# Kernel tuning notes

Hardware: AMD Instinct MI355X
Metric: run time of the kernel (lower is better)

## Reference

```python
import jax, jax.numpy as jnp
import numpy as np

N = 8192
HID = 256
LAMBDA = 1.0
MU = 1.0
DIM = 2
GC = 0.0027
L = 0.02
Y0, Y1 = 0.0, 1.0
STRESS_PRE_SCALE = 1.0
PF_PRE_SCALE = 1.0


def loading(t):
    # linear displacement loading
    return t[0]


def mlp(Ws, bs, inp):
    h = inp
    for W, b in zip(Ws[:-1], bs[:-1]):
        h = jnp.tanh(h @ W + b)
    return h @ Ws[-1] + bs[-1]


def net_u(Ws, bs, x, t):
    sol = mlp(Ws, bs, jnp.concatenate([x, t]))  # (3,)
    phi = jax.nn.sigmoid(sol[:1])               # (1,)
    ld = loading(t)
    ux = (x[1] - Y0) * (x[1] - Y1) * sol[1:2] * ld / 3.0
    uy = (x[1] - Y0) * (x[1] - Y1) * sol[2:3] * ld + (x[1] - Y0) / (Y1 - Y0) * ld
    return phi, jnp.concatenate([ux, uy])       # (1,), (2,)


def epsilon_fn(Ws, bs, x, t):
    J = jax.jacrev(lambda xx: net_u(Ws, bs, xx, t)[1])(x)  # (2,2)
    return (J + J.T) / 2.0


def psi_pos(eps):
    tr = jnp.trace(eps)
    k = LAMBDA + MU * 2.0 / DIM
    dev = eps - tr * jnp.eye(DIM, dtype=eps.dtype) / DIM
    return k * jax.nn.relu(tr) ** 2 / 2 + MU * jnp.trace(dev @ dev)


def psi_neg(eps):
    k = LAMBDA + MU * 2.0 / DIM
    return k * jax.nn.relu(-jnp.trace(eps)) ** 2 / 2


def sigma_fn(Ws, bs, x, t):
    phi, _ = net_u(Ws, bs, x, t)
    g_phi = (1 - phi[0]) ** 2 + 1e-6
    eps = epsilon_fn(Ws, bs, x, t)
    return g_phi * jax.grad(psi_pos)(eps) + jax.grad(psi_neg)(eps)


def net_stress(Ws, bs, x, t):
    def damaged(xx):
        phi, _ = net_u(Ws, bs, xx, t)
        return (1 - phi) ** 2 * sigma_fn(Ws, bs, xx, t)  # (2,2)
    D = jax.jacrev(damaged)(x)          # (2,2,2)
    return jnp.einsum('ijj->i', D) / STRESS_PRE_SCALE


def net_pf_raw(Ws, bs, x, t):
    phi, _ = net_u(Ws, bs, x, t)
    phi0 = phi[0]
    eps = epsilon_fn(Ws, bs, x, t)
    H = jax.hessian(lambda xx: net_u(Ws, bs, xx, t)[0])(x)[0]  # (2,2)
    lap_phi = jnp.trace(H)
    pf = GC * (phi0 / L - L * lap_phi) - 2 * (1 - phi0) * psi_pos(eps)
    return pf / PF_PRE_SCALE


def net_speed(Ws, bs, x, t):
    return jax.jacrev(lambda tt: net_u(Ws, bs, x, tt)[0])(t)[0, 0]


def net_pf(Ws, bs, x, t):
    pf = net_pf_raw(Ws, bs, x, t)
    dphi_dt = net_speed(Ws, bs, x, t)
    phi0 = net_u(Ws, bs, x, t)[0][0]
    mask_pos = (jnp.abs(dphi_dt) <= 1e-3) & (jnp.abs(phi0 - 1) > 1e-3)
    mask_neg = jnp.abs(phi0 - 1) <= 1e-3
    return jnp.where(mask_pos, jax.nn.relu(-pf), jnp.where(mask_neg, jax.nn.relu(pf), pf))


def net_energy(Ws, bs, x, t):
    phi0 = net_u(Ws, bs, x, t)[0][0]
    eps = epsilon_fn(Ws, bs, x, t)
    nphi = jax.jacrev(lambda xx: net_u(Ws, bs, xx, t)[0])(x)[0]  # (2,)
    return ((1 - phi0) * 2 * psi_pos(eps) + psi_neg(eps)
            + GC * (phi0 ** 2 / (2 * L) + L / 2 * jnp.sum(nphi ** 2)))


def _forward(W0, W1, W2, W3, W4, b0, b1, b2, b3, b4, x, t):
    Ws = [W0, W1, W2, W3, W4]
    bs = [b0, b1, b2, b3, b4]
    res_s = jax.vmap(net_stress, in_axes=(None, None, 0, 0))(Ws, bs, x, t)   # (N,2)
    res_pf = jax.vmap(net_pf, in_axes=(None, None, 0, 0))(Ws, bs, x, t)     # (N,)
    res_e = jax.vmap(net_energy, in_axes=(None, None, 0, 0))(Ws, bs, x, t)  # (N,)
    dphi = jax.vmap(net_speed, in_axes=(None, None, 0, 0))(Ws, bs, x, t)    # (N,)
    # component re-weighting for the vector stress residual (as in loss_pde)
    mse_res = jnp.mean(res_s ** 2, axis=0)  # (2,)
    w = jax.lax.stop_gradient(jnp.mean(mse_res) / (mse_res + 1e-6))
    r = jnp.sqrt(jnp.sum(res_s ** 2 * w[None, :], axis=-1))
    loss_stress = jnp.mean(r ** 2)
    loss_pf = jnp.mean(res_pf ** 2)
    loss_energy = jnp.log(jnp.sum(res_e))
    loss_irr = jnp.mean(jax.nn.relu(-dphi))
    return jnp.stack([loss_stress, loss_pf, loss_energy, loss_irr])


def setup_inputs() -> dict:
    key = jax.random.key(0)
    dims = [3, HID, HID, HID, HID, 3]
    ks = jax.random.split(key, 12)
    inp = {}
    for i in range(5):
        fan_in, fan_out = dims[i], dims[i + 1]
        inp[f'W{i}'] = (jax.random.normal(ks[i], (fan_in, fan_out), jnp.float32)
                        * np.sqrt(2.0 / (fan_in + fan_out)).astype(np.float32))
        inp[f'b{i}'] = jnp.zeros((fan_out,), jnp.float32)
    inp['x'] = jax.random.uniform(ks[10], (N, 2), jnp.float32, 0.0, 1.0)
    inp['t'] = jax.random.uniform(ks[11], (N, 1), jnp.float32, 0.05, 1.0)
    return inp


def reference(W0, W1, W2, W3, W4, b0, b1, b2, b3, b4, x, t):
    return _forward(W0, W1, W2, W3, W4, b0, b1, b2, b3, b4, x, t)
```

## Files before the change

kernel.cpp:

```cpp
#include <hip/hip_runtime.h>
#include <math.h>

#define N_PTS 8192
#define HIDDEN 256
#define PPB 8
#define THREADS 256
#define NBLK (N_PTS / PPB)
#define NBINS 64
#define MROWS 56
#define LDA 264
#define LDZ 260
#define BP_OFF 4096

typedef float f32x4 __attribute__((ext_vector_type(4)));
typedef short s8v  __attribute__((ext_vector_type(8)));
typedef short s4v  __attribute__((ext_vector_type(4)));

__device__ __forceinline__ unsigned short bf16_rne(float x) {
    unsigned int u = __float_as_uint(x);
    return (unsigned short)((u + 0x7FFFu + ((u >> 16) & 1u)) >> 16);
}
__device__ __forceinline__ float bf16f(unsigned short h) {
    return __uint_as_float(((unsigned int)h) << 16);
}

__global__ void pinn_pack(const float* __restrict__ W1, const float* __restrict__ W2,
                          const float* __restrict__ W3, unsigned short* __restrict__ Bp,
                          float* __restrict__ bins)
{
    if (blockIdx.x == 0) {
        bins[threadIdx.x] = 0.f;
        bins[threadIdx.x + 256] = 0.f;
    }
    const int id = blockIdx.x * 256 + threadIdx.x;
    const int lane = id & 63;
    const int nt   = (id >> 6) & 15;
    const int kc   = (id >> 10) & 7;
    const int l    = id >> 13;
    const float* W = (l == 0) ? W1 : ((l == 1) ? W2 : W3);
    const int n  = nt * 16 + (lane & 15);
    const int k0 = kc * 32 + (lane >> 4) * 8;
    unsigned short hi[8], lo[8];
    #pragma unroll
    for (int i = 0; i < 8; ++i) {
        const float x = W[(size_t)(k0 + i) * HIDDEN + n];
        const unsigned short h = bf16_rne(x);
        hi[i] = h;
        lo[i] = bf16_rne(x - bf16f(h));
    }
    const size_t bh = ((((size_t)(l * 2 + 0) * 8 + kc) * 16 + nt) * 64 + lane) * 8;
    const size_t bl = ((((size_t)(l * 2 + 1) * 8 + kc) * 16 + nt) * 64 + lane) * 8;
    *(s8v*)&Bp[bh] = *(const s8v*)hi;
    *(s8v*)&Bp[bl] = *(const s8v*)lo;
}

__global__ __launch_bounds__(THREADS, 2)
void pinn_main(const float* __restrict__ W0, const float* __restrict__ b0,
               const float* __restrict__ b1, const float* __restrict__ b2,
               const float* __restrict__ b3,
               const float* __restrict__ W4, const float* __restrict__ b4,
               const float* __restrict__ xin, const float* __restrict__ tin,
               const unsigned short* __restrict__ Bp,
               float* __restrict__ bins)
{
    __shared__ __align__(16) unsigned char LB[MROWS * LDA * 4];
    short* __restrict__ AhS = (short*)LB;
    short* __restrict__ AlS = (short*)(LB + MROWS * LDA * 2);
    float* __restrict__ Zf  = (float*)LB;

    const int tid  = threadIdx.x;
    const int lane = tid & 63;
    const int w    = tid >> 6;
    const int c    = lane & 15;
    const int g    = lane >> 4;
    const int q    = tid & 63;
    const int pp   = tid >> 6;
    const int pt0  = blockIdx.x * PPB;

    {
        const f32x4 w0 = *(const f32x4*)(W0 + q * 4);
        const f32x4 w1 = *(const f32x4*)(W0 + HIDDEN + q * 4);
        const f32x4 w2 = *(const f32x4*)(W0 + 2 * HIDDEN + q * 4);
        const f32x4 bb = *(const f32x4*)(b0 + q * 4);
        #pragma unroll
        for (int p2 = 0; p2 < 2; ++p2) {
            const int p = pp + 4 * p2;
            const float x0 = xin[(pt0 + p) * 2 + 0];
            const float x1 = xin[(pt0 + p) * 2 + 1];
            const float tt = tin[pt0 + p];
            s4v hi[7], lo[7];
            #pragma unroll
            for (int jj = 0; jj < 4; ++jj) {
                const float z  = fmaf(x0, w0[jj], fmaf(x1, w1[jj], fmaf(tt, w2[jj], bb[jj])));
                const float a  = tanhf(z);
                const float st = 1.f - a * a;
                const float m2 = -2.f * a * st;
                float v[7];
                v[0] = a;
                v[1] = st * w0[jj]; v[2] = st * w1[jj]; v[3] = st * w2[jj];
                v[4] = m2 * w0[jj] * w0[jj];
                v[5] = m2 * w0[jj] * w1[jj];
                v[6] = m2 * w1[jj] * w1[jj];
                #pragma unroll
                for (int s = 0; s < 7; ++s) {
                    const unsigned short h = bf16_rne(v[s]);
                    hi[s][jj] = (short)h;
                    lo[s][jj] = (short)bf16_rne(v[s] - bf16f(h));
                }
            }
            #pragma unroll
            for (int s = 0; s < 7; ++s) {
                const int r = 8 * s + p;
                *(s4v*)&AhS[r * LDA + q * 4] = hi[s];
                *(s4v*)&AlS[r * LDA + q * 4] = lo[s];
            }
        }
    }
    __syncthreads();

    int aoff[4];
    #pragma unroll
    for (int mt = 0; mt < 4; ++mt) {
        int arow = mt * 16 + c;
        if (arow > MROWS - 1) arow = MROWS - 1;
        aoff[mt] = arow * LDA + g * 8;
    }

    for (int l = 0; l < 3; ++l) {
        f32x4 acc[4][4];
        #pragma unroll
        for (int mt = 0; mt < 4; ++mt)
            #pragma unroll
            for (int nn = 0; nn < 4; ++nn) acc[mt][nn] = (f32x4)0.f;

        const size_t lbase = (size_t)l * 2 * 8 * 16 * 64 * 8;
        #pragma unroll
        for (int kc = 0; kc < 8; ++kc) {
            s8v ah[4], al[4];
            #pragma unroll
            for (int mt = 0; mt < 4; ++mt) {
                ah[mt] = *(const s8v*)&AhS[aoff[mt] + kc * 32];
                al[mt] = *(const s8v*)&AlS[aoff[mt] + kc * 32];
            }
            s8v bh[4], bl[4];
            #pragma unroll
            for (int nn = 0; nn < 4; ++nn) {
                const int nt = w * 4 + nn;
                const size_t oh = lbase + (((size_t)kc * 16 + nt) * 64 + lane) * 8;
                const size_t ol = oh + (size_t)8 * 16 * 64 * 8;
                bh[nn] = *(const s8v*)&Bp[oh];
                bl[nn] = *(const s8v*)&Bp[ol];
            }
            #pragma unroll
            for (int mt = 0; mt < 4; ++mt)
                #pragma unroll
                for (int nn = 0; nn < 4; ++nn) {
                    acc[mt][nn] = __builtin_amdgcn_mfma_f32_16x16x32_bf16(ah[mt], bh[nn], acc[mt][nn], 0, 0, 0);
                    acc[mt][nn] = __builtin_amdgcn_mfma_f32_16x16x32_bf16(ah[mt], bl[nn], acc[mt][nn], 0, 0, 0);
                    acc[mt][nn] = __builtin_amdgcn_mfma_f32_16x16x32_bf16(al[mt], bh[nn], acc[mt][nn], 0, 0, 0);
                }
        }
        __syncthreads();

        #pragma unroll
        for (int mt = 0; mt < 4; ++mt)
            #pragma unroll
            for (int nn = 0; nn < 4; ++nn)
                #pragma unroll
                for (int r = 0; r < 4; ++r) {
                    const int row = mt * 16 + g * 4 + r;
                    if (row < MROWS)
                        Zf[row * LDZ + w * 64 + nn * 16 + c] = acc[mt][nn][r];
                }
        __syncthreads();

        f32x4 z[2][7];
        #pragma unroll
        for (int p2 = 0; p2 < 2; ++p2) {
            const int p = pp + 4 * p2;
            #pragma unroll
            for (int s = 0; s < 7; ++s)
                z[p2][s] = *(const f32x4*)&Zf[(8 * s + p) * LDZ + q * 4];
        }
        __syncthreads();

        const float* bias = (l == 0) ? b1 : (l == 1) ? b2 : b3;
        const f32x4 bb = *(const f32x4*)(bias + q * 4);
        #pragma unroll
        for (int p2 = 0; p2 < 2; ++p2) {
            const int p = pp + 4 * p2;
            s4v hi[7], lo[7];
            f32x4 vf[7];
            #pragma unroll
            for (int jj = 0; jj < 4; ++jj) {
                const float zv = z[p2][0][jj] + bb[jj];
                const float a  = tanhf(zv);
                const float st = 1.f - a * a;
                const float m2 = -2.f * a * st;
                const float z1 = z[p2][1][jj], z2 = z[p2][2][jj], z3 = z[p2][3][jj];
                float v[7];
                v[0] = a;
                v[1] = st * z1; v[2] = st * z2; v[3] = st * z3;
                v[4] = fmaf(m2 * z1, z1, st * z[p2][4][jj]);
                v[5] = fmaf(m2 * z1, z2, st * z[p2][5][jj]);
                v[6] = fmaf(m2 * z2, z2, st * z[p2][6][jj]);
                if (l < 2) {
                    #pragma unroll
                    for (int s = 0; s < 7; ++s) {
                        const unsigned short h = bf16_rne(v[s]);
                        hi[s][jj] = (short)h;
                        lo[s][jj] = (short)bf16_rne(v[s] - bf16f(h));
                    }
                } else {
                    #pragma unroll
                    for (int s = 0; s < 7; ++s) vf[s][jj] = v[s];
                }
            }
            if (l < 2) {
                #pragma unroll
                for (int s = 0; s < 7; ++s) {
                    const int r = 8 * s + p;
                    *(s4v*)&AhS[r * LDA + q * 4] = hi[s];
                    *(s4v*)&AlS[r * LDA + q * 4] = lo[s];
                }
            } else {
                #pragma unroll
                for (int s = 0; s < 7; ++s)
                    *(f32x4*)&Zf[(8 * s + p) * LDZ + q * 4] = vf[s];
            }
        }
        __syncthreads();
    }

    const int h  = (lane >> 5);
    const int la = lane & 31;
    const int p  = w * 2 + h;

    float part[7][3];
    #pragma unroll
    for (int s = 0; s < 7; ++s)
        #pragma unroll
        for (int m = 0; m < 3; ++m) part[s][m] = 0.f;

    #pragma unroll
    for (int i = 0; i < 8; ++i) {
        const int k = la + 32 * i;
        const float w40 = W4[k * 3 + 0], w41 = W4[k * 3 + 1], w42 = W4[k * 3 + 2];
        #pragma unroll
        for (int s = 0; s < 7; ++s) {
            const float hk = Zf[(8 * s + p) * LDZ + k];
            part[s][0] = fmaf(hk, w40, part[s][0]);
            part[s][1] = fmaf(hk, w41, part[s][1]);
            part[s][2] = fmaf(hk, w42, part[s][2]);
        }
    }
    #pragma unroll
    for (int s = 0; s < 7; ++s)
        #pragma unroll
        for (int m = 0; m < 3; ++m) {
            float v = part[s][m];
            #pragma unroll
            for (int off = 16; off > 0; off >>= 1) v += __shfl_xor(v, off);
            part[s][m] = v;
        }

    const float x0 = xin[(pt0 + p) * 2 + 0];
    const float x1 = xin[(pt0 + p) * 2 + 1];
    const float tt = tin[pt0 + p];

    const float V0 = part[0][0] + b4[0];
    const float V1 = part[0][1] + b4[1];
    const float V2 = part[0][2] + b4[2];
    const float J00 = part[1][0], J01 = part[2][0], J0t = part[3][0];
    const float J10 = part[1][1], J11 = part[2][1];
    const float J20 = part[1][2], J21 = part[2][2];
    const float H000 = part[4][0], H011 = part[6][0];
    const float H100 = part[4][1], H101 = part[5][1], H111 = part[6][1];
    const float H200 = part[4][2], H201 = part[5][2], H211 = part[6][2];

    const float phi = 1.f / (1.f + expf(-V0));
    const float om  = 1.f - phi;
    const float sp  = phi * om;
    const float spp = sp * (1.f - 2.f * phi);
    const float phx0 = sp * J00, phx1 = sp * J01, dphidt = sp * J0t;
    const float lap = spp * (J00 * J00 + J01 * J01) + sp * (H000 + H011);

    const float ld = tt;
    const float qq = x1 * (x1 - 1.f), qp = 2.f * x1 - 1.f;

    const float ux0 = qq * J10 * ld * (1.f / 3.f);
    const float ux1 = (qp * V1 + qq * J11) * ld * (1.f / 3.f);
    const float uy0 = qq * J20 * ld;
    const float uy1 = (qp * V2 + qq * J21) * ld + ld;

    const float e00 = ux0, e11 = uy1, e01 = 0.5f * (ux1 + uy0);
    const float tr = e00 + e11;

    const float ux_00 = qq * H100 * ld * (1.f / 3.f);
    const float ux_01 = (qp * J10 + qq * H101) * ld * (1.f / 3.f);
    const float ux_11 = (2.f * V1 + 2.f * qp * J11 + qq * H111) * ld * (1.f / 3.f);
    const float uy_00 = qq * H200 * ld;
    const float uy_01 = (qp * J20 + qq * H201) * ld;
    const float uy_11 = (2.f * V2 + 2.f * qp * J21 + qq * H211) * ld;

    const float de00_0 = ux_00, de00_1 = ux_01;
    const float de11_0 = uy_01, de11_1 = uy_11;
    const float de01_0 = 0.5f * (ux_01 + uy_00), de01_1 = 0.5f * (ux_11 + uy_01);
    const float dtr_0 = de00_0 + de11_0, dtr_1 = de00_1 + de11_1;

    const float kk = 2.f;
    const float rtr = fmaxf(tr, 0.f), rntr = fmaxf(-tr, 0.f);
    const float Hp = (tr > 0.f) ? 1.f : 0.f, Hn = (tr < 0.f) ? 1.f : 0.f;

    const float dv = 0.5f * (e00 - e11);
    const float sp00 = kk * rtr + 2.f * dv;
    const float sp11 = kk * rtr - 2.f * dv;
    const float sp01 = 2.f * e01;
    const float snd  = -kk * rntr;

    const float dsp00_0 = kk * Hp * dtr_0 + 2.f * (de00_0 - 0.5f * dtr_0);
    const float dsp01_0 = 2.f * de01_0;
    const float dsp01_1 = 2.f * de01_1;
    const float dsp11_1 = kk * Hp * dtr_1 + 2.f * (de11_1 - 0.5f * dtr_1);
    const float dsn_0 = kk * Hn * dtr_0, dsn_1 = kk * Hn * dtr_1;

    const float cc  = om * om, gg = cc + 1e-6f;
    const float dc0 = -2.f * om * phx0, dc1 = -2.f * om * phx1;
    const float gpc = gg + cc, cg = cc * gg;

    const float res0 = dc0 * gpc * sp00 + cg * dsp00_0 + dc0 * snd + cc * dsn_0
                     + dc1 * gpc * sp01 + cg * dsp01_1;
    const float res1 = dc0 * gpc * sp01 + cg * dsp01_0
                     + dc1 * gpc * sp11 + cg * dsp11_1 + dc1 * snd + cc * dsn_1;

    const float psip = rtr * rtr + 0.5f * (e00 - e11) * (e00 - e11) + 2.f * e01 * e01;
    const float psin = rntr * rntr;

    const float GCc = 0.0027f, LL = 0.02f;
    const float pf = GCc * (phi / LL - LL * lap) - 2.f * om * psip;
    const bool maskp = (fabsf(dphidt) <= 1e-3f) && (fabsf(phi - 1.f) > 1e-3f);
    const bool maskn = fabsf(phi - 1.f) <= 1e-3f;
    const float respf = maskp ? fmaxf(-pf, 0.f) : (maskn ? fmaxf(pf, 0.f) : pf);

    const float rese = om * 2.f * psip + psin
                     + GCc * (phi * phi / (2.f * LL)
                              + 0.5f * LL * (phx0 * phx0 + phx1 * phx1));
    const float irr = fmaxf(-dphidt, 0.f);

    if (la == 0) {
        float* bin = bins + (blockIdx.x & (NBINS - 1)) * 8;
        atomicAdd(bin + 0, res0 * res0);
        atomicAdd(bin + 1, res1 * res1);
        atomicAdd(bin + 2, respf * respf);
        atomicAdd(bin + 3, rese);
        atomicAdd(bin + 4, irr);
    }
}

__global__ void pinn_finalize(const float* __restrict__ bins, float* __restrict__ out)
{
    const int lane = threadIdx.x;
    float s0 = bins[lane * 8 + 0];
    float s1 = bins[lane * 8 + 1];
    float s2 = bins[lane * 8 + 2];
    float s3 = bins[lane * 8 + 3];
    float s4 = bins[lane * 8 + 4];
    #pragma unroll
    for (int off = 32; off > 0; off >>= 1) {
        s0 += __shfl_xor(s0, off);
        s1 += __shfl_xor(s1, off);
        s2 += __shfl_xor(s2, off);
        s3 += __shfl_xor(s3, off);
        s4 += __shfl_xor(s4, off);
    }
    if (lane == 0) {
        const float inv_n = 1.f / (float)N_PTS;
        const float mse0 = s0 * inv_n, mse1 = s1 * inv_n;
        const float wm = 0.5f * (mse0 + mse1);
        out[0] = wm * mse0 / (mse0 + 1e-6f) + wm * mse1 / (mse1 + 1e-6f);
        out[1] = s2 * inv_n;
        out[2] = logf(s3);
        out[3] = s4 * inv_n;
    }
}

extern "C" void kernel_launch(void* const* d_in, const int* in_sizes, int n_in,
                              void* d_out, int out_size, void* d_ws, size_t ws_size,
                              hipStream_t stream)
{
    const float *W[5], *b[5];
    if (in_sizes[1] == HIDDEN) {
        for (int i = 0; i < 5; ++i) {
            W[i] = (const float*)d_in[2 * i];
            b[i] = (const float*)d_in[2 * i + 1];
        }
    } else {
        for (int i = 0; i < 5; ++i) {
            W[i] = (const float*)d_in[i];
            b[i] = (const float*)d_in[5 + i];
        }
    }
    const float* x = (const float*)d_in[10];
    const float* t = (const float*)d_in[11];
    float* bins = (float*)d_ws;
    unsigned short* Bp = (unsigned short*)((char*)d_ws + BP_OFF);

    pinn_pack<<<96, 256, 0, stream>>>(W[1], W[2], W[3], Bp, bins);
    pinn_main<<<NBLK, THREADS, 0, stream>>>(W[0], b[0], b[1], b[2], b[3],
                                            W[4], b[4], x, t, Bp, bins);
    pinn_finalize<<<1, 64, 0, stream>>>(bins, (float*)d_out);
}
```

Baseline: 161.6 us.

## Epilogue in MFMA registers via permuted row/K layout; fuse finalize kernel

Rows of the A tile are reordered so each lane's MFMA accumulator holds all seven derivative streams for its own points. The tanh and derivative epilogue therefore runs directly on accumulators, which removes the Zf store/reload round trip and two barriers per layer. The weight K dimension is permuted in the pack kernel and in the W4 readout so the new column order stays consistent. The separate finalize launch is replaced by a last-block-done atomic counter inside the main kernel, which adds extra LDS and a global atomic per block.

```diff
diff --git a/kernel.cpp b/kernel.cpp
--- a/kernel.cpp
+++ b/kernel.cpp
@@ -7,9 +7,9 @@
 #define THREADS 256
 #define NBLK (N_PTS / PPB)
 #define NBINS 64
-#define MROWS 56
 #define LDA 264
-#define LDZ 260
+#define AROWS 62
+#define LDZ 264
 #define BP_OFF 4096
 
 typedef float f32x4 __attribute__((ext_vector_type(4)));
@@ -22,6 +22,10 @@
 }
 __device__ __forceinline__ float bf16f(unsigned short h) {
     return __uint_as_float(((unsigned int)h) << 16);
+}
+__device__ __forceinline__ int rowof(int s, int p) {
+    return (s < 6) ? ((s >> 1) * 16 + (p >> 1) * 4 + (p & 1) * 2 + (s & 1))
+                   : (48 + (p >> 1) * 4 + (p & 1));
 }
 
 __global__ void pinn_pack(const float* __restrict__ W1, const float* __restrict__ W2,
@@ -31,6 +35,7 @@
     if (blockIdx.x == 0) {
         bins[threadIdx.x] = 0.f;
         bins[threadIdx.x + 256] = 0.f;
+        if (threadIdx.x == 0) *(unsigned*)(bins + 512) = 0u;
     }
     const int id = blockIdx.x * 256 + threadIdx.x;
     const int lane = id & 63;
@@ -39,11 +44,12 @@
     const int l    = id >> 13;
     const float* W = (l == 0) ? W1 : ((l == 1) ? W2 : W3);
     const int n  = nt * 16 + (lane & 15);
-    const int k0 = kc * 32 + (lane >> 4) * 8;
     unsigned short hi[8], lo[8];
     #pragma unroll
     for (int i = 0; i < 8; ++i) {
-        const float x = W[(size_t)(k0 + i) * HIDDEN + n];
+        const int kslot = kc * 32 + (lane >> 4) * 8 + i;
+        const int korig = ((kslot >> 6) & 3) * 64 + (kslot & 3) * 16 + ((kslot >> 2) & 15);
+        const float x = W[(size_t)korig * HIDDEN + n];
         const unsigned short h = bf16_rne(x);
         hi[i] = h;
         lo[i] = bf16_rne(x - bf16f(h));
@@ -61,11 +67,11 @@
                const float* __restrict__ W4, const float* __restrict__ b4,
                const float* __restrict__ xin, const float* __restrict__ tin,
                const unsigned short* __restrict__ Bp,
-               float* __restrict__ bins)
+               float* __restrict__ bins, float* __restrict__ out)
 {
-    __shared__ __align__(16) unsigned char LB[MROWS * LDA * 4];
+    __shared__ __align__(16) unsigned char LB[65472];
     short* __restrict__ AhS = (short*)LB;
-    short* __restrict__ AlS = (short*)(LB + MROWS * LDA * 2);
+    short* __restrict__ AlS = (short*)(LB + AROWS * LDA * 2);
     float* __restrict__ Zf  = (float*)LB;
 
     const int tid  = threadIdx.x;
@@ -73,58 +79,70 @@
     const int w    = tid >> 6;
     const int c    = lane & 15;
     const int g    = lane >> 4;
-    const int q    = tid & 63;
-    const int pp   = tid >> 6;
     const int pt0  = blockIdx.x * PPB;
+    unsigned* cnt  = (unsigned*)(bins + 512);
 
     {
-        const f32x4 w0 = *(const f32x4*)(W0 + q * 4);
-        const f32x4 w1 = *(const f32x4*)(W0 + HIDDEN + q * 4);
-        const f32x4 w2 = *(const f32x4*)(W0 + 2 * HIDDEN + q * 4);
-        const f32x4 bb = *(const f32x4*)(b0 + q * 4);
-        #pragma unroll
-        for (int p2 = 0; p2 < 2; ++p2) {
-            const int p = pp + 4 * p2;
+        const int c0i = tid & 15, w0i = (tid >> 4) & 3, pp = tid >> 6;
+        float w0v[4], w1v[4], w2v[4], bbv[4];
+        #pragma unroll
+        for (int nn = 0; nn < 4; ++nn) {
+            const int j = w0i * 64 + 16 * nn + c0i;
+            w0v[nn] = W0[j]; w1v[nn] = W0[HIDDEN + j]; w2v[nn] = W0[2 * HIDDEN + j];
+            bbv[nn] = b0[j];
+        }
+        const int sbase = 4 * (c0i + 16 * w0i);
+        #pragma unroll
+        for (int e = 0; e < 2; ++e) {
+            const int p = pp + 4 * e;
             const float x0 = xin[(pt0 + p) * 2 + 0];
             const float x1 = xin[(pt0 + p) * 2 + 1];
             const float tt = tin[pt0 + p];
             s4v hi[7], lo[7];
             #pragma unroll
-            for (int jj = 0; jj < 4; ++jj) {
-                const float z  = fmaf(x0, w0[jj], fmaf(x1, w1[jj], fmaf(tt, w2[jj], bb[jj])));
+            for (int nn = 0; nn < 4; ++nn) {
+                const float z  = fmaf(x0, w0v[nn], fmaf(x1, w1v[nn], fmaf(tt, w2v[nn], bbv[nn])));
                 const float a  = tanhf(z);
                 const float st = 1.f - a * a;
                 const float m2 = -2.f * a * st;
                 float v[7];
                 v[0] = a;
-                v[1] = st * w0[jj]; v[2] = st * w1[jj]; v[3] = st * w2[jj];
-                v[4] = m2 * w0[jj] * w0[jj];
-                v[5] = m2 * w0[jj] * w1[jj];
-                v[6] = m2 * w1[jj] * w1[jj];
+                v[1] = st * w0v[nn]; v[2] = st * w1v[nn]; v[3] = st * w2v[nn];
+                v[4] = m2 * w0v[nn] * w0v[nn];
+                v[5] = m2 * w0v[nn] * w1v[nn];
+                v[6] = m2 * w1v[nn] * w1v[nn];
                 #pragma unroll
                 for (int s = 0; s < 7; ++s) {
                     const unsigned short h = bf16_rne(v[s]);
-                    hi[s][jj] = (short)h;
-                    lo[s][jj] = (short)bf16_rne(v[s] - bf16f(h));
+                    hi[s][nn] = (short)h;
+                    lo[s][nn] = (short)bf16_rne(v[s] - bf16f(h));
                 }
             }
             #pragma unroll
             for (int s = 0; s < 7; ++s) {
-                const int r = 8 * s + p;
-                *(s4v*)&AhS[r * LDA + q * 4] = hi[s];
-                *(s4v*)&AlS[r * LDA + q * 4] = lo[s];
-            }
+                const int r = rowof(s, p);
+                *(s4v*)&AhS[r * LDA + sbase] = hi[s];
+                *(s4v*)&AlS[r * LDA + sbase] = lo[s];
+            }
+        }
+        if (pp == 0) {
+            const s4v z4 = {0, 0, 0, 0};
+            #pragma unroll
+            for (int b = 0; b < 3; ++b)
+                #pragma unroll
+                for (int d = 2; d < 4; ++d) {
+                    const int r = 48 + 4 * b + d;
+                    *(s4v*)&AhS[r * LDA + sbase] = z4;
+                    *(s4v*)&AlS[r * LDA + sbase] = z4;
+                }
         }
     }
     __syncthreads();
 
     int aoff[4];
     #pragma unroll
-    for (int mt = 0; mt < 4; ++mt) {
-        int arow = mt * 16 + c;
-        if (arow > MROWS - 1) arow = MROWS - 1;
-        aoff[mt] = arow * LDA + g * 8;
-    }
+    for (int mt = 0; mt < 3; ++mt) aoff[mt] = (16 * mt + c) * LDA + g * 8;
+    aoff[3] = (48 + ((c >= 14) ? 0 : c)) * LDA + g * 8;
 
     for (int l = 0; l < 3; ++l) {
         f32x4 acc[4][4];
@@ -162,71 +180,54 @@
         }
         __syncthreads();
 
-        #pragma unroll
-        for (int mt = 0; mt < 4; ++mt)
-            #pragma unroll
-            for (int nn = 0; nn < 4; ++nn)
-                #pragma unroll
-                for (int r = 0; r < 4; ++r) {
-                    const int row = mt * 16 + g * 4 + r;
-                    if (row < MROWS)
-                        Zf[row * LDZ + w * 64 + nn * 16 + c] = acc[mt][nn][r];
-                }
-        __syncthreads();
-
-        f32x4 z[2][7];
-        #pragma unroll
-        for (int p2 = 0; p2 < 2; ++p2) {
-            const int p = pp + 4 * p2;
-            #pragma unroll
-            for (int s = 0; s < 7; ++s)
-                z[p2][s] = *(const f32x4*)&Zf[(8 * s + p) * LDZ + q * 4];
-        }
-        __syncthreads();
-
         const float* bias = (l == 0) ? b1 : (l == 1) ? b2 : b3;
-        const f32x4 bb = *(const f32x4*)(bias + q * 4);
-        #pragma unroll
-        for (int p2 = 0; p2 < 2; ++p2) {
-            const int p = pp + 4 * p2;
-            s4v hi[7], lo[7];
-            f32x4 vf[7];
-            #pragma unroll
-            for (int jj = 0; jj < 4; ++jj) {
-                const float zv = z[p2][0][jj] + bb[jj];
-                const float a  = tanhf(zv);
+        float bbv[4];
+        #pragma unroll
+        for (int nn = 0; nn < 4; ++nn) bbv[nn] = bias[64 * w + 16 * nn + c];
+        const int sbase = 4 * (c + 16 * w);
+
+        #pragma unroll
+        for (int e = 0; e < 2; ++e) {
+            const int p = 2 * g + e;
+            float v[7][4];
+            #pragma unroll
+            for (int nn = 0; nn < 4; ++nn) {
+                const float z0 = acc[0][nn][2 * e + 0] + bbv[nn];
+                const float z1 = acc[0][nn][2 * e + 1];
+                const float z2 = acc[1][nn][2 * e + 0];
+                const float z3 = acc[1][nn][2 * e + 1];
+                const float z4 = acc[2][nn][2 * e + 0];
+                const float z5 = acc[2][nn][2 * e + 1];
+                const float z6 = acc[3][nn][e];
+                const float a  = tanhf(z0);
                 const float st = 1.f - a * a;
                 const float m2 = -2.f * a * st;
-                const float z1 = z[p2][1][jj], z2 = z[p2][2][jj], z3 = z[p2][3][jj];
-                float v[7];
-                v[0] = a;
-                v[1] = st * z1; v[2] = st * z2; v[3] = st * z3;
-                v[4] = fmaf(m2 * z1, z1, st * z[p2][4][jj]);
-                v[5] = fmaf(m2 * z1, z2, st * z[p2][5][jj]);
-                v[6] = fmaf(m2 * z2, z2, st * z[p2][6][jj]);
-                if (l < 2) {
-                    #pragma unroll
-                    for (int s = 0; s < 7; ++s) {
-                        const unsigned short h = bf16_rne(v[s]);
-                        hi[s][jj] = (short)h;
-                        lo[s][jj] = (short)bf16_rne(v[s] - bf16f(h));
-                    }
-                } else {
-                    #pragma unroll
-                    for (int s = 0; s < 7; ++s) vf[s][jj] = v[s];
-                }
+                v[0][nn] = a;
+                v[1][nn] = st * z1; v[2][nn] = st * z2; v[3][nn] = st * z3;
+                v[4][nn] = fmaf(m2 * z1, z1, st * z4);
+                v[5][nn] = fmaf(m2 * z1, z2, st * z5);
+                v[6][nn] = fmaf(m2 * z2, z2, st * z6);
             }
             if (l < 2) {
                 #pragma unroll
                 for (int s = 0; s < 7; ++s) {
-                    const int r = 8 * s + p;
-                    *(s4v*)&AhS[r * LDA + q * 4] = hi[s];
-                    *(s4v*)&AlS[r * LDA + q * 4] = lo[s];
+                    s4v hi, lo;
+                    #pragma unroll
+                    for (int nn = 0; nn < 4; ++nn) {
+                        const unsigned short h = bf16_rne(v[s][nn]);
+                        hi[nn] = (short)h;
+                        lo[nn] = (short)bf16_rne(v[s][nn] - bf16f(h));
+                    }
+                    const int r = rowof(s, p);
+                    *(s4v*)&AhS[r * LDA + sbase] = hi;
+                    *(s4v*)&AlS[r * LDA + sbase] = lo;
                 }
             } else {
                 #pragma unroll
-                for (int s = 0; s < 7; ++s)
-                    *(f32x4*)&Zf[(8 * s + p) * LDZ + q * 4] = vf[s];
+                for (int s = 0; s < 7; ++s) {
+                    f32x4 vv = {v[s][0], v[s][1], v[s][2], v[s][3]};
+                    *(f32x4*)&Zf[(8 * s + p) * LDZ + sbase] = vv;
+                }
             }
         }
         __syncthreads();
@@ -244,11 +245,12 @@
 
     #pragma unroll
     for (int i = 0; i < 8; ++i) {
-        const int k = la + 32 * i;
-        const float w40 = W4[k * 3 + 0], w41 = W4[k * 3 + 1], w42 = W4[k * 3 + 2];
+        const int kslot = la + 32 * i;
+        const int korig = ((kslot >> 6) & 3) * 64 + (kslot & 3) * 16 + ((kslot >> 2) & 15);
+        const float w40 = W4[korig * 3 + 0], w41 = W4[korig * 3 + 1], w42 = W4[korig * 3 + 2];
         #pragma unroll
         for (int s = 0; s < 7; ++s) {
-            const float hk = Zf[(8 * s + p) * LDZ + k];
+            const float hk = Zf[(8 * s + p) * LDZ + kslot];
             part[s][0] = fmaf(hk, w40, part[s][0]);
             part[s][1] = fmaf(hk, w41, part[s][1]);
             part[s][2] = fmaf(hk, w42, part[s][2]);
@@ -355,32 +357,39 @@
         atomicAdd(bin + 3, rese);
         atomicAdd(bin + 4, irr);
     }
-}
-
-__global__ void pinn_finalize(const float* __restrict__ bins, float* __restrict__ out)
-{
-    const int lane = threadIdx.x;
-    float s0 = bins[lane * 8 + 0];
-    float s1 = bins[lane * 8 + 1];
-    float s2 = bins[lane * 8 + 2];
-    float s3 = bins[lane * 8 + 3];
-    float s4 = bins[lane * 8 + 4];
-    #pragma unroll
-    for (int off = 32; off > 0; off >>= 1) {
-        s0 += __shfl_xor(s0, off);
-        s1 += __shfl_xor(s1, off);
-        s2 += __shfl_xor(s2, off);
-        s3 += __shfl_xor(s3, off);
-        s4 += __shfl_xor(s4, off);
-    }
-    if (lane == 0) {
-        const float inv_n = 1.f / (float)N_PTS;
-        const float mse0 = s0 * inv_n, mse1 = s1 * inv_n;
-        const float wm = 0.5f * (mse0 + mse1);
-        out[0] = wm * mse0 / (mse0 + 1e-6f) + wm * mse1 / (mse1 + 1e-6f);
-        out[1] = s2 * inv_n;
-        out[2] = logf(s3);
-        out[3] = s4 * inv_n;
+
+    __syncthreads();
+    volatile unsigned* flg = (volatile unsigned*)(LB + 65024);
+    if (tid == 0) {
+        const unsigned old = atomicAdd(cnt, 1u);
+        *flg = old;
+    }
+    __syncthreads();
+    if (*flg == NBLK - 1) {
+        if (tid < 64) {
+            float s0 = atomicAdd(&bins[tid * 8 + 0], 0.f);
+            float s1 = atomicAdd(&bins[tid * 8 + 1], 0.f);
+            float s2 = atomicAdd(&bins[tid * 8 + 2], 0.f);
+            float s3 = atomicAdd(&bins[tid * 8 + 3], 0.f);
+            float s4 = atomicAdd(&bins[tid * 8 + 4], 0.f);
+            #pragma unroll
+            for (int off = 32; off > 0; off >>= 1) {
+                s0 += __shfl_xor(s0, off);
+                s1 += __shfl_xor(s1, off);
+                s2 += __shfl_xor(s2, off);
+                s3 += __shfl_xor(s3, off);
+                s4 += __shfl_xor(s4, off);
+            }
+            if (tid == 0) {
+                const float inv_n = 1.f / (float)N_PTS;
+                const float mse0 = s0 * inv_n, mse1 = s1 * inv_n;
+                const float wm = 0.5f * (mse0 + mse1);
+                out[0] = wm * mse0 / (mse0 + 1e-6f) + wm * mse1 / (mse1 + 1e-6f);
+                out[1] = s2 * inv_n;
+                out[2] = logf(s3);
+                out[3] = s4 * inv_n;
+            }
+        }
     }
 }
 
@@ -407,6 +416,6 @@
 
     pinn_pack<<<96, 256, 0, stream>>>(W[1], W[2], W[3], Bp, bins);
     pinn_main<<<NBLK, THREADS, 0, stream>>>(W[0], b[0], b[1], b[2], b[3],
-                                            W[4], b[4], x, t, Bp, bins);
-    pinn_finalize<<<1, 64, 0, stream>>>(bins, (float*)d_out);
-}
+                                            W[4], b[4], x, t, Bp, bins,
+                                            (float*)d_out);
+}
```

Result: faster. 155.1 us (-4.0%).
